# Performance work log

Hardware: AMD Instinct MI355X
Metric: run time of the kernel (lower is better)

Reference implementation:

```python
import jax, jax.numpy as jnp
import numpy as np

N, E = 50000, 800000
F_IN, F_H, H, F_OUT = 128, 16, 8, 64
NEG_SLOPE = 0.2
LN_EPS = 1e-5


def setup_inputs() -> dict:
    key = jax.random.key(0)
    ks = jax.random.split(key, 8)
    g = lambda k, shp, fan: (jax.random.normal(k, shp, jnp.float32) / np.sqrt(fan).astype(np.float32))
    return {
        "x": jax.random.normal(ks[0], (N, F_IN), jnp.float32),
        "edge_index": jax.random.randint(ks[1], (2, E), 0, N, jnp.int32),
        "Wl1": g(ks[2], (F_IN, H * F_H), F_IN),
        "Wr1": g(ks[3], (F_IN, H * F_H), F_IN),
        "att1": g(ks[4], (H, F_H), F_H),
        "bias1": jnp.zeros((H * F_H,), jnp.float32),
        "g1": jnp.ones((H * F_H,), jnp.float32),
        "b1": jnp.zeros((H * F_H,), jnp.float32),
        "Wl2": g(ks[5], (H * F_H, F_OUT), H * F_H),
        "Wr2": g(ks[6], (H * F_H, F_OUT), H * F_H),
        "att2": g(ks[7], (1, F_OUT), F_OUT),
        "bias2": jnp.zeros((F_OUT,), jnp.float32),
        "g2": jnp.ones((F_OUT,), jnp.float32),
        "b2": jnp.zeros((F_OUT,), jnp.float32),
    }


def gatv2_conv(x, edge_index, Wl, Wr, att, bias, concat):
    """PyG GATv2Conv (eval mode, dropout inactive).
    message m_e = leaky_relu(xl[src] + xr[dst]); alpha = softmax_dst(<m_e, att>);
    out_i = sum_{e: dst=i} alpha_e * xl[src_e]. Concat or mean over heads, + bias.
    """
    n = x.shape[0]
    h, c = att.shape
    src, dst = edge_index[0], edge_index[1]
    xl = (x @ Wl).reshape(n, h, c)  # source transform (lin_l)
    xr = (x @ Wr).reshape(n, h, c)  # target transform (lin_r)
    e = jax.nn.leaky_relu(xl[src] + xr[dst], NEG_SLOPE)  # [E,h,c]
    a = jnp.einsum("ehc,hc->eh", e, att)  # [E,h]
    # segment softmax over destination node
    m = jax.ops.segment_max(a, dst, num_segments=n)  # [n,h]
    m = jnp.where(jnp.isfinite(m), m, 0.0)  # isolated nodes -> -inf guard
    ea = jnp.exp(a - m[dst])
    s = jax.ops.segment_sum(ea, dst, num_segments=n)
    alpha = ea / (s[dst] + 1e-16)  # [E,h]
    out = jax.ops.segment_sum(xl[src] * alpha[..., None], dst, num_segments=n)  # [n,h,c]
    out = out.reshape(n, h * c) if concat else out.mean(axis=1)
    return out + bias


def layer_norm(x, gamma, beta):
    mu = x.mean(-1, keepdims=True)
    var = ((x - mu) ** 2).mean(-1, keepdims=True)
    return (x - mu) * jax.lax.rsqrt(var + LN_EPS) * gamma + beta


def reference(x, edge_index, Wl1, Wr1, att1, bias1, g1, b1,
              Wl2, Wr2, att2, bias2, g2, b2):
    h1 = gatv2_conv(x, edge_index, Wl1, Wr1, att1, bias1, concat=True)
    h1 = jax.nn.elu(layer_norm(h1, g1, b1))
    h2 = gatv2_conv(h1, edge_index, Wl2, Wr2, att2, bias2, concat=False)
    return layer_norm(h2, g2, b2)
```

## Files before the change

kernel.cpp:

```cpp
#include <hip/hip_runtime.h>
#include <hip/hip_bf16.h>
#include <math.h>

typedef short s16x8 __attribute__((ext_vector_type(8)));
typedef float f32x4 __attribute__((ext_vector_type(4)));
typedef float f32x2 __attribute__((ext_vector_type(2)));

__device__ __forceinline__ float bflo(unsigned u) { return __uint_as_float(u << 16); }
__device__ __forceinline__ float bfhi(unsigned u) { return __uint_as_float(u & 0xffff0000u); }
__device__ __forceinline__ unsigned short f2bf(float f) {
    __hip_bfloat16 h = __float2bfloat16(f);
    return __builtin_bit_cast(unsigned short, h);
}
__device__ __forceinline__ f32x4 mfma_bf16(s16x8 a, s16x8 b, f32x4 c) {
    asm("v_mfma_f32_16x16x32_bf16 %0, %1, %2, %0" : "+v"(c) : "v"(a), "v"(b));
    return c;
}
__device__ __forceinline__ f32x2 unpk2(unsigned u) { return (f32x2){bflo(u), bfhi(u)}; }
__device__ __forceinline__ f32x2 plrelu(f32x2 x) {
    return __builtin_elementwise_max(x, x * 0.2f);
}
template <int CTRL>
__device__ __forceinline__ float dpp_add(float v) {
    int y = __builtin_amdgcn_update_dpp(0, __builtin_bit_cast(int, v), CTRL, 0xf, 0xf, true);
    return v + __builtin_bit_cast(float, y);
}
__device__ __forceinline__ float red8(float p) {
    p = dpp_add<0xB1>(p); p = dpp_add<0x4E>(p); return dpp_add<0x141>(p);
}
__device__ __forceinline__ float red16(float p) {
    p = dpp_add<0xB1>(p); p = dpp_add<0x4E>(p);
    p = dpp_add<0x141>(p); return dpp_add<0x140>(p);
}

__global__ void degree_rank_kernel(const int* __restrict__ dst, int* __restrict__ deg,
                                   int* __restrict__ rank, int E) {
    int e = blockIdx.x * blockDim.x + threadIdx.x;
    if (e < E) rank[e] = atomicAdd(&deg[dst[e]], 1);
}

__global__ __launch_bounds__(1024) void scan_part_kernel(const int* __restrict__ deg,
                                                         int* __restrict__ off,
                                                         int* __restrict__ bsum, int n) {
    __shared__ int wsum[16];
    int t = threadIdx.x, lane = t & 63, w = t >> 6;
    int i = blockIdx.x * 4096 + t * 4;
    int4 v = make_int4(0, 0, 0, 0);
    if (i + 3 < n) v = *reinterpret_cast<const int4*>(&deg[i]);
    else {
        if (i < n) v.x = deg[i];
        if (i + 1 < n) v.y = deg[i + 1];
        if (i + 2 < n) v.z = deg[i + 2];
    }
    int tsum = v.x + v.y + v.z + v.w;
    int x = tsum;
    #pragma unroll
    for (int d = 1; d < 64; d <<= 1) { int y = __shfl_up(x, d); if (lane >= d) x += y; }
    if (lane == 63) wsum[w] = x;
    __syncthreads();
    if (t < 16) {
        int y = wsum[t];
        #pragma unroll
        for (int d = 1; d < 16; d <<= 1) { int z = __shfl_up(y, d); if (t >= d) y += z; }
        wsum[t] = y;
    }
    __syncthreads();
    int excl = ((w == 0) ? 0 : wsum[w - 1]) + (x - tsum);
    if (i < n) off[i] = excl;
    if (i + 1 < n) off[i + 1] = excl + v.x;
    if (i + 2 < n) off[i + 2] = excl + v.x + v.y;
    if (i + 3 < n) off[i + 3] = excl + v.x + v.y + v.z;
    __syncthreads();
    if (t == 1023) bsum[blockIdx.x] = wsum[15];
}

__global__ __launch_bounds__(64) void scan_tops_kernel(const int* __restrict__ bsum,
                                                       int* __restrict__ tops,
                                                       int* __restrict__ off,
                                                       int nblk, int n) {
    int t = threadIdx.x;
    int v = (t < nblk) ? bsum[t] : 0;
    int x = v;
    #pragma unroll
    for (int d = 1; d < 64; d <<= 1) { int y = __shfl_up(x, d); if (t >= d) x += y; }
    if (t < nblk) tops[t] = x - v;
    if (t == 63) off[n] = x;
}

__global__ __launch_bounds__(1024) void scan_add_kernel(int* __restrict__ off,
                                                        const int* __restrict__ tops, int n) {
    int b = blockIdx.x;
    int base = tops[b];
    int i = b * 4096 + threadIdx.x * 4;
    if (i + 3 < n) {
        int4 v = *reinterpret_cast<const int4*>(&off[i]);
        v.x += base; v.y += base; v.z += base; v.w += base;
        *reinterpret_cast<int4*>(&off[i]) = v;
    } else {
        if (i < n) off[i] += base;
        if (i + 1 < n) off[i + 1] += base;
        if (i + 2 < n) off[i + 2] += base;
    }
}

__global__ void scatter_kernel(const int* __restrict__ src, const int* __restrict__ dst,
                               const int* __restrict__ off, const int* __restrict__ rank,
                               int* __restrict__ ssrc, int E) {
    int e = blockIdx.x * blockDim.x + threadIdx.x;
    if (e < E) {
        int d = dst[e];
        ssrc[off[d] + rank[e]] = src[e];
    }
}

__global__ void wt_prep_kernel(const float* __restrict__ Wl1, const float* __restrict__ Wr1,
                               const float* __restrict__ Wl2, const float* __restrict__ Wr2,
                               unsigned short* __restrict__ Wt1, unsigned short* __restrict__ Wt2) {
    int idx = blockIdx.x * 256 + threadIdx.x;
    if (idx < 256 * 128) {
        int n = idx >> 7, k = idx & 127;
        float v = (n < 128) ? Wl1[k * 128 + n] : Wr1[k * 128 + (n - 128)];
        Wt1[idx] = f2bf(v);
    } else if (idx < 256 * 128 + 128 * 128) {
        int j = idx - 256 * 128;
        int n = j >> 7, k = j & 127;
        float v = (n < 64) ? Wl2[k * 64 + n] : Wr2[k * 64 + (n - 64)];
        Wt2[j] = f2bf(v);
    }
}

template <int NOUT, bool AFP32>
__global__ __launch_bounds__(256) void mfma_gemm_kernel(
    const void* __restrict__ A, const unsigned short* __restrict__ Wt,
    unsigned short* __restrict__ Cl, unsigned short* __restrict__ Cr, int nrows) {
    constexpr int HALF = NOUT / 2;
    constexpr int CT = NOUT / 64;
    __shared__ unsigned short As[64 * 128];
    int t = threadIdx.x, lane = t & 63, wave = t >> 6;
    int row_base = blockIdx.x * 64;
    int rows_here = nrows - row_base;
    #pragma unroll
    for (int it = 0; it < 4; ++it) {
        int q = it * 256 + t;
        int r = q >> 4, c8 = q & 15;
        int su = r * 16 + (c8 ^ (r & 7));
        s16x8 v = {0, 0, 0, 0, 0, 0, 0, 0};
        if (r < rows_here) {
            if (AFP32) {
                const float4* g = reinterpret_cast<const float4*>(
                    (const float*)A + ((size_t)(row_base + r)) * 128 + c8 * 8);
                float4 v0 = g[0], v1 = g[1];
                union { s16x8 s; unsigned short u[8]; } pk;
                pk.u[0] = f2bf(v0.x); pk.u[1] = f2bf(v0.y);
                pk.u[2] = f2bf(v0.z); pk.u[3] = f2bf(v0.w);
                pk.u[4] = f2bf(v1.x); pk.u[5] = f2bf(v1.y);
                pk.u[6] = f2bf(v1.z); pk.u[7] = f2bf(v1.w);
                v = pk.s;
            } else {
                v = *reinterpret_cast<const s16x8*>(
                    (const unsigned short*)A + ((size_t)(row_base + r)) * 128 + c8 * 8);
            }
        }
        reinterpret_cast<s16x8*>(As)[su] = v;
    }
    __syncthreads();
    int m16 = lane & 15, kg = lane >> 4;
    int colw = wave * (NOUT / 4);
    s16x8 bfr[CT][4];
    const s16x8* Wt16 = reinterpret_cast<const s16x8*>(Wt);
    #pragma unroll
    for (int ct = 0; ct < CT; ++ct)
        #pragma unroll
        for (int ks = 0; ks < 4; ++ks)
            bfr[ct][ks] = Wt16[(size_t)(colw + ct * 16 + m16) * 16 + ks * 4 + kg];
    f32x4 acc[4][CT];
    #pragma unroll
    for (int rt = 0; rt < 4; ++rt)
        #pragma unroll
        for (int ct = 0; ct < CT; ++ct) acc[rt][ct] = (f32x4){0.f, 0.f, 0.f, 0.f};
    const s16x8* As16 = reinterpret_cast<const s16x8*>(As);
    int sw = m16 & 7;
    #pragma unroll
    for (int rt = 0; rt < 4; ++rt) {
        int abase = (rt * 16 + m16) * 16;
        #pragma unroll
        for (int ks = 0; ks < 4; ++ks) {
            s16x8 af = As16[abase + ((ks * 4 + kg) ^ sw)];
            #pragma unroll
            for (int ct = 0; ct < CT; ++ct)
                acc[rt][ct] = mfma_bf16(bfr[ct][ks], af, acc[rt][ct]);
        }
    }
    #pragma unroll
    for (int rt = 0; rt < 4; ++rt) {
        int row = row_base + rt * 16 + m16;
        if (row < nrows) {
            #pragma unroll
            for (int ct = 0; ct < CT; ++ct) {
                int n0 = colw + ct * 16 + kg * 4;
                unsigned short* Cp = (n0 < HALF) ? (Cl + n0) : (Cr + (n0 - HALF));
                ushort4 w4;
                w4.x = f2bf(acc[rt][ct][0]);
                w4.y = f2bf(acc[rt][ct][1]);
                w4.z = f2bf(acc[rt][ct][2]);
                w4.w = f2bf(acc[rt][ct][3]);
                *reinterpret_cast<ushort4*>(&Cp[(size_t)row * HALF]) = w4;
            }
        }
    }
}

__global__ __launch_bounds__(256) void gat1_kernel(
    const unsigned short* __restrict__ xl, const unsigned short* __restrict__ xr,
    const int* __restrict__ off, const int* __restrict__ ssrc,
    const float* __restrict__ att, const float* __restrict__ bias,
    const float* __restrict__ gamma, const float* __restrict__ beta,
    unsigned short* __restrict__ out, int n) {
    int lane = threadIdx.x & 63;
    int node = blockIdx.x * 4 + (threadIdx.x >> 6);
    if (node >= n) return;
    int h = lane >> 3;
    int i0 = h * 16 + ((lane & 7) << 1);
    f32x2 xrp = unpk2(*reinterpret_cast<const unsigned*>(xr + (size_t)node * 128 + i0));
    f32x2 atp = {att[i0], att[i0 + 1]};
    float s = 0.f;
    f32x2 ac = {0.f, 0.f};
    int beg = off[node], end = off[node + 1];
    int i = beg;
    for (; i + 4 <= end; i += 4) {
        int e0 = ssrc[i], e1 = ssrc[i + 1], e2 = ssrc[i + 2], e3 = ssrc[i + 3];
        unsigned u0 = *reinterpret_cast<const unsigned*>(xl + (size_t)e0 * 128 + i0);
        unsigned u1 = *reinterpret_cast<const unsigned*>(xl + (size_t)e1 * 128 + i0);
        unsigned u2 = *reinterpret_cast<const unsigned*>(xl + (size_t)e2 * 128 + i0);
        unsigned u3 = *reinterpret_cast<const unsigned*>(xl + (size_t)e3 * 128 + i0);
        f32x2 x0 = unpk2(u0), x1 = unpk2(u1), x2 = unpk2(u2), x3 = unpk2(u3);
        f32x2 q0 = plrelu(x0 + xrp) * atp;
        f32x2 q1 = plrelu(x1 + xrp) * atp;
        f32x2 q2 = plrelu(x2 + xrp) * atp;
        f32x2 q3 = plrelu(x3 + xrp) * atp;
        float p0 = q0.x + q0.y, p1 = q1.x + q1.y;
        float p2 = q2.x + q2.y, p3 = q3.x + q3.y;
        p0 = dpp_add<0xB1>(p0); p1 = dpp_add<0xB1>(p1);
        p2 = dpp_add<0xB1>(p2); p3 = dpp_add<0xB1>(p3);
        p0 = dpp_add<0x4E>(p0); p1 = dpp_add<0x4E>(p1);
        p2 = dpp_add<0x4E>(p2); p3 = dpp_add<0x4E>(p3);
        p0 = dpp_add<0x141>(p0); p1 = dpp_add<0x141>(p1);
        p2 = dpp_add<0x141>(p2); p3 = dpp_add<0x141>(p3);
        float w0 = __expf(fminf(p0, 60.f));
        float w1 = __expf(fminf(p1, 60.f));
        float w2 = __expf(fminf(p2, 60.f));
        float w3 = __expf(fminf(p3, 60.f));
        s += (w0 + w1) + (w2 + w3);
        ac += w0 * x0 + w1 * x1;
        ac += w2 * x2 + w3 * x3;
    }
    for (; i < end; ++i) {
        int e = ssrc[i];
        f32x2 xv = unpk2(*reinterpret_cast<const unsigned*>(xl + (size_t)e * 128 + i0));
        f32x2 q = plrelu(xv + xrp) * atp;
        float p = red8(q.x + q.y);
        float w = __expf(fminf(p, 60.f));
        s += w; ac += w * xv;
    }
    float inv = 1.f / (s + 1e-16f);
    float o0 = ac.x * inv + bias[i0];
    float o1 = ac.y * inv + bias[i0 + 1];
    float tsum = o0 + o1;
    #pragma unroll
    for (int d = 1; d < 64; d <<= 1) tsum += __shfl_xor(tsum, d);
    float mu = tsum * (1.f / 128.f);
    float d0 = o0 - mu, d1 = o1 - mu;
    float vsum = d0 * d0 + d1 * d1;
    #pragma unroll
    for (int d = 1; d < 64; d <<= 1) vsum += __shfl_xor(vsum, d);
    float rs = rsqrtf(vsum * (1.f / 128.f) + 1e-5f);
    float y0 = d0 * rs * gamma[i0] + beta[i0];
    float y1 = d1 * rs * gamma[i0 + 1] + beta[i0 + 1];
    y0 = y0 > 0.f ? y0 : expm1f(y0);
    y1 = y1 > 0.f ? y1 : expm1f(y1);
    unsigned pk = (unsigned)f2bf(y0) | ((unsigned)f2bf(y1) << 16);
    *reinterpret_cast<unsigned*>(out + (size_t)node * 128 + i0) = pk;
}

__global__ __launch_bounds__(256) void gat2_kernel(
    const unsigned short* __restrict__ xl, const unsigned short* __restrict__ xr,
    const int* __restrict__ off, const int* __restrict__ ssrc,
    const float* __restrict__ att, const float* __restrict__ bias,
    const float* __restrict__ gamma, const float* __restrict__ beta,
    float* __restrict__ out, int n) {
    int lane = threadIdx.x & 63;
    int node = blockIdx.x * 4 + (threadIdx.x >> 6);
    if (node >= n) return;
    int j2 = lane >> 4;
    int q = lane & 15;
    int fb = q * 4;
    uint2 uxr = *reinterpret_cast<const uint2*>(xr + (size_t)node * 64 + fb);
    f32x2 xr0 = unpk2(uxr.x), xr1 = unpk2(uxr.y);
    float4 at = *reinterpret_cast<const float4*>(att + fb);
    f32x2 at0 = {at.x, at.y}, at1 = {at.z, at.w};
    float s = 0.f;
    f32x2 ac0 = {0.f, 0.f}, ac1 = {0.f, 0.f};
    int beg = off[node], end = off[node + 1];
    for (int base = beg; base < end; base += 4) {
        int idx = base + j2;
        bool valid = idx < end;
        int e = ssrc[valid ? idx : beg];
        uint2 u = *reinterpret_cast<const uint2*>(xl + (size_t)e * 64 + fb);
        f32x2 x0 = unpk2(u.x), x1 = unpk2(u.y);
        f32x2 g0 = plrelu(x0 + xr0) * at0;
        f32x2 g1 = plrelu(x1 + xr1) * at1;
        f32x2 gs = g0 + g1;
        float p = red16(gs.x + gs.y);
        float w = valid ? __expf(fminf(p, 60.f)) : 0.f;
        s += w;
        ac0 += w * x0;
        ac1 += w * x1;
    }
    #pragma unroll
    for (int d = 16; d <= 32; d <<= 1) {
        s += __shfl_xor(s, d);
        ac0.x += __shfl_xor(ac0.x, d); ac0.y += __shfl_xor(ac0.y, d);
        ac1.x += __shfl_xor(ac1.x, d); ac1.y += __shfl_xor(ac1.y, d);
    }
    float inv = 1.f / (s + 1e-16f);
    float4 bi = *reinterpret_cast<const float4*>(bias + fb);
    float o0 = ac0.x * inv + bi.x;
    float o1 = ac0.y * inv + bi.y;
    float o2 = ac1.x * inv + bi.z;
    float o3 = ac1.y * inv + bi.w;
    float tsum = red16((o0 + o1) + (o2 + o3));
    float mu = tsum * (1.f / 64.f);
    float d0 = o0 - mu, d1 = o1 - mu, d2 = o2 - mu, d3 = o3 - mu;
    float vs = red16((d0 * d0 + d1 * d1) + (d2 * d2 + d3 * d3));
    float rs = rsqrtf(vs * (1.f / 64.f) + 1e-5f);
    if (j2 == 0) {
        float4 ga = *reinterpret_cast<const float4*>(gamma + fb);
        float4 be = *reinterpret_cast<const float4*>(beta + fb);
        float4 y;
        y.x = d0 * rs * ga.x + be.x;
        y.y = d1 * rs * ga.y + be.y;
        y.z = d2 * rs * ga.z + be.z;
        y.w = d3 * rs * ga.w + be.w;
        *reinterpret_cast<float4*>(out + (size_t)node * 64 + fb) = y;
    }
}

extern "C" void kernel_launch(void* const* d_in, const int* in_sizes, int n_in,
                              void* d_out, int out_size, void* d_ws, size_t ws_size,
                              hipStream_t stream) {
    const float* x = (const float*)d_in[0];
    const int* ei = (const int*)d_in[1];
    const float* Wl1 = (const float*)d_in[2];
    const float* Wr1 = (const float*)d_in[3];
    const float* att1 = (const float*)d_in[4];
    const float* bias1 = (const float*)d_in[5];
    const float* g1 = (const float*)d_in[6];
    const float* b1 = (const float*)d_in[7];
    const float* Wl2 = (const float*)d_in[8];
    const float* Wr2 = (const float*)d_in[9];
    const float* att2 = (const float*)d_in[10];
    const float* bias2 = (const float*)d_in[11];
    const float* g2 = (const float*)d_in[12];
    const float* b2 = (const float*)d_in[13];
    float* out = (float*)d_out;

    const int N = in_sizes[0] / 128;
    const int E = in_sizes[1] / 2;
    const int* src = ei;
    const int* dstp = ei + E;

    char* p = (char*)d_ws;
    auto alloc = [&](size_t bytes) -> char* {
        char* r = p;
        p += (bytes + 255) & ~(size_t)255;
        return r;
    };
    int* deg = (int*)alloc((size_t)N * 4);
    int* rank = (int*)alloc((size_t)E * 4);
    int* off = (int*)alloc((size_t)(N + 1) * 4);
    int* ssrc = (int*)alloc((size_t)E * 4);
    int* bsum = (int*)alloc(64 * 4);
    int* tops = (int*)alloc(64 * 4);
    unsigned short* Wt1 = (unsigned short*)alloc(256 * 128 * 2);
    unsigned short* Wt2 = (unsigned short*)alloc(128 * 128 * 2);
    unsigned short* bufA = (unsigned short*)alloc((size_t)N * 128 * 2);
    unsigned short* bufB = (unsigned short*)alloc((size_t)N * 128 * 2);
    unsigned short* h1u = (unsigned short*)alloc((size_t)N * 128 * 2);

    const int nblk = (N + 4095) / 4096;

    hipMemsetAsync(deg, 0, (size_t)N * 4, stream);
    degree_rank_kernel<<<(E + 255) / 256, 256, 0, stream>>>(dstp, deg, rank, E);
    wt_prep_kernel<<<(256 * 128 + 128 * 128 + 255) / 256, 256, 0, stream>>>(
        Wl1, Wr1, Wl2, Wr2, Wt1, Wt2);
    scan_part_kernel<<<nblk, 1024, 0, stream>>>(deg, off, bsum, N);
    scan_tops_kernel<<<1, 64, 0, stream>>>(bsum, tops, off, nblk, N);
    scan_add_kernel<<<nblk, 1024, 0, stream>>>(off, tops, N);
    scatter_kernel<<<(E + 255) / 256, 256, 0, stream>>>(src, dstp, off, rank, ssrc, E);

    int gblocks = (N + 63) / 64;
    mfma_gemm_kernel<256, true><<<gblocks, 256, 0, stream>>>(x, Wt1, bufA, bufB, N);
    gat1_kernel<<<(N + 3) / 4, 256, 0, stream>>>(bufA, bufB, off, ssrc, att1, bias1, g1, b1, h1u, N);
    mfma_gemm_kernel<128, false><<<gblocks, 256, 0, stream>>>(h1u, Wt2, bufA, bufB, N);
    gat2_kernel<<<(N + 3) / 4, 256, 0, stream>>>(bufA, bufB, off, ssrc, att2, bias2, g2, b2, out, N);
}
```

Baseline: 268.1 us.

## Fuse preprocessing launches and co-schedule degree counting with first GEMM

Folds the degree-buffer memset into the weight-prep kernel and merges the atomic degree/rank pass with the first-layer GEMM into one launch that splits blocks by index. The separate tops-scan kernel is dropped; each scan_add block sums the preceding block totals serially. The GAT kernels switch from four-node 256-thread blocks to one node per 64-thread block. The aim is fewer kernel launches and letting the atomic-bound and MFMA-bound work overlap on the device, at the cost of a mixed-role kernel that allocates shared memory for the degree blocks and a serial prefix loop.

```diff
diff --git a/kernel.cpp b/kernel.cpp
--- a/kernel.cpp
+++ b/kernel.cpp
@@ -33,111 +33,46 @@
     p = dpp_add<0x141>(p); return dpp_add<0x140>(p);
 }
 
-__global__ void degree_rank_kernel(const int* __restrict__ dst, int* __restrict__ deg,
-                                   int* __restrict__ rank, int E) {
-    int e = blockIdx.x * blockDim.x + threadIdx.x;
-    if (e < E) rank[e] = atomicAdd(&deg[dst[e]], 1);
-}
-
-__global__ __launch_bounds__(1024) void scan_part_kernel(const int* __restrict__ deg,
-                                                         int* __restrict__ off,
-                                                         int* __restrict__ bsum, int n) {
-    __shared__ int wsum[16];
-    int t = threadIdx.x, lane = t & 63, w = t >> 6;
-    int i = blockIdx.x * 4096 + t * 4;
-    int4 v = make_int4(0, 0, 0, 0);
-    if (i + 3 < n) v = *reinterpret_cast<const int4*>(&deg[i]);
-    else {
-        if (i < n) v.x = deg[i];
-        if (i + 1 < n) v.y = deg[i + 1];
-        if (i + 2 < n) v.z = deg[i + 2];
-    }
-    int tsum = v.x + v.y + v.z + v.w;
-    int x = tsum;
-    #pragma unroll
-    for (int d = 1; d < 64; d <<= 1) { int y = __shfl_up(x, d); if (lane >= d) x += y; }
-    if (lane == 63) wsum[w] = x;
-    __syncthreads();
-    if (t < 16) {
-        int y = wsum[t];
-        #pragma unroll
-        for (int d = 1; d < 16; d <<= 1) { int z = __shfl_up(y, d); if (t >= d) y += z; }
-        wsum[t] = y;
-    }
-    __syncthreads();
-    int excl = ((w == 0) ? 0 : wsum[w - 1]) + (x - tsum);
-    if (i < n) off[i] = excl;
-    if (i + 1 < n) off[i + 1] = excl + v.x;
-    if (i + 2 < n) off[i + 2] = excl + v.x + v.y;
-    if (i + 3 < n) off[i + 3] = excl + v.x + v.y + v.z;
-    __syncthreads();
-    if (t == 1023) bsum[blockIdx.x] = wsum[15];
-}
-
-__global__ __launch_bounds__(64) void scan_tops_kernel(const int* __restrict__ bsum,
-                                                       int* __restrict__ tops,
-                                                       int* __restrict__ off,
-                                                       int nblk, int n) {
-    int t = threadIdx.x;
-    int v = (t < nblk) ? bsum[t] : 0;
-    int x = v;
-    #pragma unroll
-    for (int d = 1; d < 64; d <<= 1) { int y = __shfl_up(x, d); if (t >= d) x += y; }
-    if (t < nblk) tops[t] = x - v;
-    if (t == 63) off[n] = x;
-}
-
-__global__ __launch_bounds__(1024) void scan_add_kernel(int* __restrict__ off,
-                                                        const int* __restrict__ tops, int n) {
-    int b = blockIdx.x;
-    int base = tops[b];
-    int i = b * 4096 + threadIdx.x * 4;
-    if (i + 3 < n) {
-        int4 v = *reinterpret_cast<const int4*>(&off[i]);
-        v.x += base; v.y += base; v.z += base; v.w += base;
-        *reinterpret_cast<int4*>(&off[i]) = v;
-    } else {
-        if (i < n) off[i] += base;
-        if (i + 1 < n) off[i + 1] += base;
-        if (i + 2 < n) off[i + 2] += base;
-    }
-}
-
-__global__ void scatter_kernel(const int* __restrict__ src, const int* __restrict__ dst,
-                               const int* __restrict__ off, const int* __restrict__ rank,
-                               int* __restrict__ ssrc, int E) {
-    int e = blockIdx.x * blockDim.x + threadIdx.x;
-    if (e < E) {
-        int d = dst[e];
-        ssrc[off[d] + rank[e]] = src[e];
-    }
-}
-
-__global__ void wt_prep_kernel(const float* __restrict__ Wl1, const float* __restrict__ Wr1,
-                               const float* __restrict__ Wl2, const float* __restrict__ Wr2,
-                               unsigned short* __restrict__ Wt1, unsigned short* __restrict__ Wt2) {
+__global__ void prep_kernel(const float* __restrict__ Wl1, const float* __restrict__ Wr1,
+                            const float* __restrict__ Wl2, const float* __restrict__ Wr2,
+                            unsigned short* __restrict__ Wt1, unsigned short* __restrict__ Wt2,
+                            int* __restrict__ deg, int n) {
     int idx = blockIdx.x * 256 + threadIdx.x;
     if (idx < 256 * 128) {
-        int n = idx >> 7, k = idx & 127;
-        float v = (n < 128) ? Wl1[k * 128 + n] : Wr1[k * 128 + (n - 128)];
+        int c = idx >> 7, k = idx & 127;
+        float v = (c < 128) ? Wl1[k * 128 + c] : Wr1[k * 128 + (c - 128)];
         Wt1[idx] = f2bf(v);
     } else if (idx < 256 * 128 + 128 * 128) {
         int j = idx - 256 * 128;
-        int n = j >> 7, k = j & 127;
-        float v = (n < 64) ? Wl2[k * 64 + n] : Wr2[k * 64 + (n - 64)];
+        int c = j >> 7, k = j & 127;
+        float v = (c < 64) ? Wl2[k * 64 + c] : Wr2[k * 64 + (c - 64)];
         Wt2[j] = f2bf(v);
-    }
-}
-
-template <int NOUT, bool AFP32>
-__global__ __launch_bounds__(256) void mfma_gemm_kernel(
-    const void* __restrict__ A, const unsigned short* __restrict__ Wt,
+    } else {
+        int z = idx - (256 * 128 + 128 * 128);
+        int i = z * 4;
+        if (i + 3 < n) *reinterpret_cast<int4*>(&deg[i]) = make_int4(0, 0, 0, 0);
+        else {
+            if (i < n) deg[i] = 0;
+            if (i + 1 < n) deg[i + 1] = 0;
+            if (i + 2 < n) deg[i + 2] = 0;
+        }
+    }
+}
+
+__global__ __launch_bounds__(256) void degree_gemm_kernel(
+    const int* __restrict__ dst, int* __restrict__ deg, int* __restrict__ rank, int E,
+    int dblocks,
+    const float* __restrict__ A, const unsigned short* __restrict__ Wt,
     unsigned short* __restrict__ Cl, unsigned short* __restrict__ Cr, int nrows) {
-    constexpr int HALF = NOUT / 2;
-    constexpr int CT = NOUT / 64;
     __shared__ unsigned short As[64 * 128];
+    if (blockIdx.x < (unsigned)dblocks) {
+        int e = blockIdx.x * 256 + threadIdx.x;
+        if (e < E) rank[e] = atomicAdd(&deg[dst[e]], 1);
+        return;
+    }
+    constexpr int NOUT = 256, HALF = 128, CT = 4;
     int t = threadIdx.x, lane = t & 63, wave = t >> 6;
-    int row_base = blockIdx.x * 64;
+    int row_base = (blockIdx.x - dblocks) * 64;
     int rows_here = nrows - row_base;
     #pragma unroll
     for (int it = 0; it < 4; ++it) {
@@ -146,20 +81,15 @@
         int su = r * 16 + (c8 ^ (r & 7));
         s16x8 v = {0, 0, 0, 0, 0, 0, 0, 0};
         if (r < rows_here) {
-            if (AFP32) {
-                const float4* g = reinterpret_cast<const float4*>(
-                    (const float*)A + ((size_t)(row_base + r)) * 128 + c8 * 8);
-                float4 v0 = g[0], v1 = g[1];
-                union { s16x8 s; unsigned short u[8]; } pk;
-                pk.u[0] = f2bf(v0.x); pk.u[1] = f2bf(v0.y);
-                pk.u[2] = f2bf(v0.z); pk.u[3] = f2bf(v0.w);
-                pk.u[4] = f2bf(v1.x); pk.u[5] = f2bf(v1.y);
-                pk.u[6] = f2bf(v1.z); pk.u[7] = f2bf(v1.w);
-                v = pk.s;
-            } else {
-                v = *reinterpret_cast<const s16x8*>(
-                    (const unsigned short*)A + ((size_t)(row_base + r)) * 128 + c8 * 8);
-            }
+            const float4* g = reinterpret_cast<const float4*>(
+                A + ((size_t)(row_base + r)) * 128 + c8 * 8);
+            float4 v0 = g[0], v1 = g[1];
+            union { s16x8 s; unsigned short u[8]; } pk;
+            pk.u[0] = f2bf(v0.x); pk.u[1] = f2bf(v0.y);
+            pk.u[2] = f2bf(v0.z); pk.u[3] = f2bf(v0.w);
+            pk.u[4] = f2bf(v1.x); pk.u[5] = f2bf(v1.y);
+            pk.u[6] = f2bf(v1.z); pk.u[7] = f2bf(v1.w);
+            v = pk.s;
         }
         reinterpret_cast<s16x8*>(As)[su] = v;
     }
@@ -210,14 +140,147 @@
     }
 }
 
-__global__ __launch_bounds__(256) void gat1_kernel(
+__global__ __launch_bounds__(1024) void scan_part_kernel(const int* __restrict__ deg,
+                                                         int* __restrict__ off,
+                                                         int* __restrict__ bsum, int n) {
+    __shared__ int wsum[16];
+    int t = threadIdx.x, lane = t & 63, w = t >> 6;
+    int i = blockIdx.x * 4096 + t * 4;
+    int4 v = make_int4(0, 0, 0, 0);
+    if (i + 3 < n) v = *reinterpret_cast<const int4*>(&deg[i]);
+    else {
+        if (i < n) v.x = deg[i];
+        if (i + 1 < n) v.y = deg[i + 1];
+        if (i + 2 < n) v.z = deg[i + 2];
+    }
+    int tsum = v.x + v.y + v.z + v.w;
+    int x = tsum;
+    #pragma unroll
+    for (int d = 1; d < 64; d <<= 1) { int y = __shfl_up(x, d); if (lane >= d) x += y; }
+    if (lane == 63) wsum[w] = x;
+    __syncthreads();
+    if (t < 16) {
+        int y = wsum[t];
+        #pragma unroll
+        for (int d = 1; d < 16; d <<= 1) { int z = __shfl_up(y, d); if (t >= d) y += z; }
+        wsum[t] = y;
+    }
+    __syncthreads();
+    int excl = ((w == 0) ? 0 : wsum[w - 1]) + (x - tsum);
+    if (i < n) off[i] = excl;
+    if (i + 1 < n) off[i + 1] = excl + v.x;
+    if (i + 2 < n) off[i + 2] = excl + v.x + v.y;
+    if (i + 3 < n) off[i + 3] = excl + v.x + v.y + v.z;
+    __syncthreads();
+    if (t == 1023) bsum[blockIdx.x] = wsum[15];
+}
+
+__global__ __launch_bounds__(1024) void scan_add_kernel(int* __restrict__ off,
+                                                        const int* __restrict__ bsum,
+                                                        int nblk, int n) {
+    int b = blockIdx.x;
+    int base = 0;
+    for (int j = 0; j < b; ++j) base += bsum[j];
+    int i = b * 4096 + threadIdx.x * 4;
+    if (i + 3 < n) {
+        int4 v = *reinterpret_cast<const int4*>(&off[i]);
+        v.x += base; v.y += base; v.z += base; v.w += base;
+        *reinterpret_cast<int4*>(&off[i]) = v;
+    } else {
+        if (i < n) off[i] += base;
+        if (i + 1 < n) off[i + 1] += base;
+        if (i + 2 < n) off[i + 2] += base;
+    }
+    if (b == 0 && threadIdx.x == 0) {
+        int tot = 0;
+        for (int j = 0; j < nblk; ++j) tot += bsum[j];
+        off[n] = tot;
+    }
+}
+
+__global__ void scatter_kernel(const int* __restrict__ src, const int* __restrict__ dst,
+                               const int* __restrict__ off, const int* __restrict__ rank,
+                               int* __restrict__ ssrc, int E) {
+    int e = blockIdx.x * blockDim.x + threadIdx.x;
+    if (e < E) {
+        int d = dst[e];
+        ssrc[off[d] + rank[e]] = src[e];
+    }
+}
+
+__global__ __launch_bounds__(256) void mfma_gemm128_kernel(
+    const unsigned short* __restrict__ A, const unsigned short* __restrict__ Wt,
+    unsigned short* __restrict__ Cl, unsigned short* __restrict__ Cr, int nrows) {
+    constexpr int NOUT = 128, HALF = 64, CT = 2;
+    __shared__ unsigned short As[64 * 128];
+    int t = threadIdx.x, lane = t & 63, wave = t >> 6;
+    int row_base = blockIdx.x * 64;
+    int rows_here = nrows - row_base;
+    #pragma unroll
+    for (int it = 0; it < 4; ++it) {
+        int q = it * 256 + t;
+        int r = q >> 4, c8 = q & 15;
+        int su = r * 16 + (c8 ^ (r & 7));
+        s16x8 v = {0, 0, 0, 0, 0, 0, 0, 0};
+        if (r < rows_here)
+            v = *reinterpret_cast<const s16x8*>(A + ((size_t)(row_base + r)) * 128 + c8 * 8);
+        reinterpret_cast<s16x8*>(As)[su] = v;
+    }
+    __syncthreads();
+    int m16 = lane & 15, kg = lane >> 4;
+    int colw = wave * (NOUT / 4);
+    s16x8 bfr[CT][4];
+    const s16x8* Wt16 = reinterpret_cast<const s16x8*>(Wt);
+    #pragma unroll
+    for (int ct = 0; ct < CT; ++ct)
+        #pragma unroll
+        for (int ks = 0; ks < 4; ++ks)
+            bfr[ct][ks] = Wt16[(size_t)(colw + ct * 16 + m16) * 16 + ks * 4 + kg];
+    f32x4 acc[4][CT];
+    #pragma unroll
+    for (int rt = 0; rt < 4; ++rt)
+        #pragma unroll
+        for (int ct = 0; ct < CT; ++ct) acc[rt][ct] = (f32x4){0.f, 0.f, 0.f, 0.f};
+    const s16x8* As16 = reinterpret_cast<const s16x8*>(As);
+    int sw = m16 & 7;
+    #pragma unroll
+    for (int rt = 0; rt < 4; ++rt) {
+        int abase = (rt * 16 + m16) * 16;
+        #pragma unroll
+        for (int ks = 0; ks < 4; ++ks) {
+            s16x8 af = As16[abase + ((ks * 4 + kg) ^ sw)];
+            #pragma unroll
+            for (int ct = 0; ct < CT; ++ct)
+                acc[rt][ct] = mfma_bf16(bfr[ct][ks], af, acc[rt][ct]);
+        }
+    }
+    #pragma unroll
+    for (int rt = 0; rt < 4; ++rt) {
+        int row = row_base + rt * 16 + m16;
+        if (row < nrows) {
+            #pragma unroll
+            for (int ct = 0; ct < CT; ++ct) {
+                int n0 = colw + ct * 16 + kg * 4;
+                unsigned short* Cp = (n0 < HALF) ? (Cl + n0) : (Cr + (n0 - HALF));
+                ushort4 w4;
+                w4.x = f2bf(acc[rt][ct][0]);
+                w4.y = f2bf(acc[rt][ct][1]);
+                w4.z = f2bf(acc[rt][ct][2]);
+                w4.w = f2bf(acc[rt][ct][3]);
+                *reinterpret_cast<ushort4*>(&Cp[(size_t)row * HALF]) = w4;
+            }
+        }
+    }
+}
+
+__global__ __launch_bounds__(64) void gat1_kernel(
     const unsigned short* __restrict__ xl, const unsigned short* __restrict__ xr,
     const int* __restrict__ off, const int* __restrict__ ssrc,
     const float* __restrict__ att, const float* __restrict__ bias,
     const float* __restrict__ gamma, const float* __restrict__ beta,
     unsigned short* __restrict__ out, int n) {
-    int lane = threadIdx.x & 63;
-    int node = blockIdx.x * 4 + (threadIdx.x >> 6);
+    int lane = threadIdx.x;
+    int node = blockIdx.x;
     if (node >= n) return;
     int h = lane >> 3;
     int i0 = h * 16 + ((lane & 7) << 1);
@@ -282,14 +345,14 @@
     *reinterpret_cast<unsigned*>(out + (size_t)node * 128 + i0) = pk;
 }
 
-__global__ __launch_bounds__(256) void gat2_kernel(
+__global__ __launch_bounds__(64) void gat2_kernel(
     const unsigned short* __restrict__ xl, const unsigned short* __restrict__ xr,
     const int* __restrict__ off, const int* __restrict__ ssrc,
     const float* __restrict__ att, const float* __restrict__ bias,
     const float* __restrict__ gamma, const float* __restrict__ beta,
     float* __restrict__ out, int n) {
-    int lane = threadIdx.x & 63;
-    int node = blockIdx.x * 4 + (threadIdx.x >> 6);
+    int lane = threadIdx.x;
+    int node = blockIdx.x;
     if (node >= n) return;
     int j2 = lane >> 4;
     int q = lane & 15;
@@ -380,7 +443,6 @@
     int* off = (int*)alloc((size_t)(N + 1) * 4);
     int* ssrc = (int*)alloc((size_t)E * 4);
     int* bsum = (int*)alloc(64 * 4);
-    int* tops = (int*)alloc(64 * 4);
     unsigned short* Wt1 = (unsigned short*)alloc(256 * 128 * 2);
     unsigned short* Wt2 = (unsigned short*)alloc(128 * 128 * 2);
     unsigned short* bufA = (unsigned short*)alloc((size_t)N * 128 * 2);
@@ -388,19 +450,18 @@
     unsigned short* h1u = (unsigned short*)alloc((size_t)N * 128 * 2);
 
     const int nblk = (N + 4095) / 4096;
-
-    hipMemsetAsync(deg, 0, (size_t)N * 4, stream);
-    degree_rank_kernel<<<(E + 255) / 256, 256, 0, stream>>>(dstp, deg, rank, E);
-    wt_prep_kernel<<<(256 * 128 + 128 * 128 + 255) / 256, 256, 0, stream>>>(
-        Wl1, Wr1, Wl2, Wr2, Wt1, Wt2);
+    const int gblocks = (N + 63) / 64;
+    const int dblocks = (E + 255) / 256;
+    const int prep_threads = 256 * 128 + 128 * 128 + (N + 3) / 4;
+
+    prep_kernel<<<(prep_threads + 255) / 256, 256, 0, stream>>>(
+        Wl1, Wr1, Wl2, Wr2, Wt1, Wt2, deg, N);
+    degree_gemm_kernel<<<dblocks + gblocks, 256, 0, stream>>>(
+        dstp, deg, rank, E, dblocks, x, Wt1, bufA, bufB, N);
     scan_part_kernel<<<nblk, 1024, 0, stream>>>(deg, off, bsum, N);
-    scan_tops_kernel<<<1, 64, 0, stream>>>(bsum, tops, off, nblk, N);
-    scan_add_kernel<<<nblk, 1024, 0, stream>>>(off, tops, N);
+    scan_add_kernel<<<nblk, 1024, 0, stream>>>(off, bsum, nblk, N);
     scatter_kernel<<<(E + 255) / 256, 256, 0, stream>>>(src, dstp, off, rank, ssrc, E);
-
-    int gblocks = (N + 63) / 64;
-    mfma_gemm_kernel<256, true><<<gblocks, 256, 0, stream>>>(x, Wt1, bufA, bufB, N);
-    gat1_kernel<<<(N + 3) / 4, 256, 0, stream>>>(bufA, bufB, off, ssrc, att1, bias1, g1, b1, h1u, N);
-    mfma_gemm_kernel<128, false><<<gblocks, 256, 0, stream>>>(h1u, Wt2, bufA, bufB, N);
-    gat2_kernel<<<(N + 3) / 4, 256, 0, stream>>>(bufA, bufB, off, ssrc, att2, bias2, g2, b2, out, N);
-}
+    gat1_kernel<<<N, 64, 0, stream>>>(bufA, bufB, off, ssrc, att1, bias1, g1, b1, h1u, N);
+    mfma_gemm128_kernel<<<gblocks, 256, 0, stream>>>(h1u, Wt2, bufA, bufB, N);
+    gat2_kernel<<<N, 64, 0, stream>>>(bufA, bufB, off, ssrc, att2, bias2, g2, b2, out, N);
+}
```

New measurement: 252.9 us. 5.6% less time.
